# Performance work log

Measured on AMD Instinct MI355X. Metric: run time of the kernel, lower is better.

## Reference

```python
import jax, jax.numpy as jnp
import numpy as np

D = 256
FF = 1024
NH = 8
BZ, TL = 8, 1024
L, Hs, Ws = 1, 64, 64


def _linear(x, w, b):
    # torch nn.Linear convention: w is [out, in]
    return x @ w.T + b


def _ln(x, g, b, eps=1e-5):
    m = x.mean(-1, keepdims=True)
    v = ((x - m) ** 2).mean(-1, keepdims=True)
    return (x - m) / jnp.sqrt(v + eps) * g + b


def setup_inputs() -> dict:
    key = jax.random.key(0)
    ks = jax.random.split(key, 16)
    s = 0.02
    inp = {
        "tgt": jax.random.normal(ks[0], (BZ, TL, D), jnp.float32),
        "reference_points": jax.random.uniform(ks[1], (BZ, TL, 2), jnp.float32),
        "srcs": jax.random.normal(ks[2], (BZ, L, D, Hs, Ws), jnp.float32),
        "posemb_2d": jax.random.normal(ks[3], (BZ, TL, D), jnp.float32),
        # self-attn (nn.MultiheadAttention) params
        "in_proj_w": jax.random.normal(ks[4], (3 * D, D), jnp.float32) * s,
        "in_proj_b": jnp.zeros((3 * D,), jnp.float32),
        "out_proj_w": jax.random.normal(ks[5], (D, D), jnp.float32) * s,
        "out_proj_b": jnp.zeros((D,), jnp.float32),
        # hand-rolled cross-attn linears (q, k, v, out)
        "lin_q_w": jax.random.normal(ks[6], (D, D), jnp.float32) * s,
        "lin_q_b": jnp.zeros((D,), jnp.float32),
        "lin_k_w": jax.random.normal(ks[7], (D, D), jnp.float32) * s,
        "lin_k_b": jnp.zeros((D,), jnp.float32),
        "lin_v_w": jax.random.normal(ks[8], (D, D), jnp.float32) * s,
        "lin_v_b": jnp.zeros((D,), jnp.float32),
        "lin_o_w": jax.random.normal(ks[9], (D, D), jnp.float32) * s,
        "lin_o_b": jnp.zeros((D,), jnp.float32),
        # layer norms
        "norm1_g": jnp.ones((D,), jnp.float32),
        "norm1_b": jnp.zeros((D,), jnp.float32),
        "norm2_g": jnp.ones((D,), jnp.float32),
        "norm2_b": jnp.zeros((D,), jnp.float32),
        # FFN
        "ffn_w1": jax.random.normal(ks[10], (FF, D), jnp.float32) * s,
        "ffn_b1": jnp.zeros((FF,), jnp.float32),
        "ffn_w2": jax.random.normal(ks[11], (D, FF), jnp.float32) * s,
        "ffn_b2": jnp.zeros((D,), jnp.float32),
        "ffn_norm_g": jnp.ones((D,), jnp.float32),
        "ffn_norm_b": jnp.zeros((D,), jnp.float32),
    }
    return inp


def reference(tgt, reference_points, srcs, posemb_2d,
              in_proj_w, in_proj_b, out_proj_w, out_proj_b,
              lin_q_w, lin_q_b, lin_k_w, lin_k_b, lin_v_w, lin_v_b,
              lin_o_w, lin_o_b,
              norm1_g, norm1_b, norm2_g, norm2_b,
              ffn_w1, ffn_b1, ffn_w2, ffn_b2, ffn_norm_g, ffn_norm_b):
    bz, tl, c = tgt.shape
    nh = NH
    dh = c // nh
    scale = dh ** -0.5

    # ---- self-attention (nn.MultiheadAttention math) ----
    qk = tgt + posemb_2d  # q = k = with_pos_embed(tgt, posemb_2d_)
    wq, wk, wv = in_proj_w[:c], in_proj_w[c:2 * c], in_proj_w[2 * c:]
    bq, bk, bv = in_proj_b[:c], in_proj_b[c:2 * c], in_proj_b[2 * c:]
    qp = _linear(qk, wq, bq).reshape(bz, tl, nh, dh)
    kp = _linear(qk, wk, bk).reshape(bz, tl, nh, dh)
    vp = _linear(tgt, wv, bv).reshape(bz, tl, nh, dh)
    att = jax.nn.softmax(jnp.einsum('bqhd,bkhd->bhqk', qp * scale, kp), axis=-1)
    sa = jnp.einsum('bhqk,bkhd->bqhd', att, vp).reshape(bz, tl, c)
    sa = _linear(sa, out_proj_w, out_proj_b)
    tgt = _ln(tgt + sa, norm2_g, norm2_b)

    # ---- hand-rolled cross attention ----
    bz_, l, c_, h, w = srcs.shape
    s = jnp.transpose(srcs.reshape(bz_ * l, c_, h, w), (0, 2, 3, 1)).reshape(bz_ * l, h * w, c_)
    query = _linear(tgt, lin_q_w, lin_q_b)          # [bz, tl, c]
    key = _linear(s, lin_k_w, lin_k_b)              # [bz*l, hw, c]
    value = _linear(s, lin_v_w, lin_v_b)
    affinity = jax.nn.softmax(jnp.einsum('bqc,bkc->bqk', query, key), axis=-1)  # no 1/sqrt(d) scale, faithful
    tgt2 = _linear(jnp.einsum('bqk,bkc->bqc', affinity, value), lin_o_w, lin_o_b)
    tgt = _ln(tgt + tgt2, norm1_g, norm1_b)

    # ---- FFN ----
    src2 = _linear(jax.nn.relu(_linear(tgt, ffn_w1, ffn_b1)), ffn_w2, ffn_b2)
    tgt = _ln(tgt + src2, ffn_norm_g, ffn_norm_b)
    return tgt
```

## Files before the change

kernel.cpp:

```cpp
#include <hip/hip_runtime.h>
#include <hip/hip_bf16.h>
#include <math.h>

typedef __attribute__((ext_vector_type(8))) __bf16 bf16x8;
typedef __attribute__((ext_vector_type(4))) __bf16 bf16x4;
typedef __attribute__((ext_vector_type(2))) __bf16 bf16x2;
typedef __attribute__((ext_vector_type(4))) float  f32x4;

#define MFMA16(a,b,c) __builtin_amdgcn_mfma_f32_16x16x32_bf16((a),(b),(c),0,0,0)

__device__ __forceinline__ unsigned pack2bf(float a, float b){
  bf16x2 t; t[0] = (__bf16)a; t[1] = (__bf16)b;
  return __builtin_bit_cast(unsigned, t);
}
__device__ __forceinline__ int perm1(int r){ return ((r<<2)|(r>>1)) & 7; }

__device__ __forceinline__ bf16x8 cvt8(const float4& a, const float4& b){
  bf16x8 h;
  h[0]=(__bf16)a.x; h[1]=(__bf16)a.y; h[2]=(__bf16)a.z; h[3]=(__bf16)a.w;
  h[4]=(__bf16)b.x; h[5]=(__bf16)b.y; h[6]=(__bf16)b.z; h[7]=(__bf16)b.w;
  return h;
}

template<int BM, bool RELU, int OUTMODE, int AMODE>
__global__ __launch_bounds__(256) void gemm_bt(
    const void* __restrict__ Av, const float* __restrict__ A2,
    const float* __restrict__ W,
    const float* __restrict__ bias, void* __restrict__ Cv,
    int M, int N, int K, int ldc, int coff, float oscale)
{
  constexpr int MT = BM/32;
  constexpr int PASSES = BM/64;
  __shared__ __align__(16) __bf16 As[BM][72];
  __shared__ __align__(16) __bf16 Bs[64][72];

  const int tid  = threadIdx.x;
  const int wid  = tid >> 6;
  const int lane = tid & 63;
  const int wr   = wid >> 1;
  const int wc   = wid & 1;
  const int lq   = lane & 15;
  const int lk8  = (lane >> 4) << 3;
  const int rb   = (lane >> 4) << 2;

  const int m0 = blockIdx.x * BM;
  const int n0 = blockIdx.y * 64;

  const int sr = tid >> 2;
  const int sc = (tid & 3) << 4;

  f32x4 acc[MT][2];
  #pragma unroll
  for (int i=0;i<MT;i++)
    #pragma unroll
    for (int j=0;j<2;j++) acc[i][j] = f32x4{0.f,0.f,0.f,0.f};

  for (int k0=0; k0<K; k0+=64){
    __syncthreads();
    #pragma unroll
    for (int p=0;p<PASSES;p++){
      const int row = sr + p*64;
      if (AMODE == 2){
        const __bf16* ap = (const __bf16*)Av + (size_t)(m0+row)*K + k0 + sc;
        *(bf16x8*)&As[row][sc]   = *(const bf16x8*)(ap);
        *(bf16x8*)&As[row][sc+8] = *(const bf16x8*)(ap + 8);
      } else {
        const float* ap = (const float*)Av + (size_t)(m0+row)*K + k0 + sc;
        float4 a0 = *(const float4*)(ap);
        float4 a1 = *(const float4*)(ap+4);
        float4 a2 = *(const float4*)(ap+8);
        float4 a3 = *(const float4*)(ap+12);
        if (AMODE == 1){
          const float* bp = A2 + (size_t)(m0+row)*K + k0 + sc;
          const float4 b0 = *(const float4*)(bp);
          const float4 b1 = *(const float4*)(bp+4);
          const float4 b2 = *(const float4*)(bp+8);
          const float4 b3 = *(const float4*)(bp+12);
          a0.x+=b0.x; a0.y+=b0.y; a0.z+=b0.z; a0.w+=b0.w;
          a1.x+=b1.x; a1.y+=b1.y; a1.z+=b1.z; a1.w+=b1.w;
          a2.x+=b2.x; a2.y+=b2.y; a2.z+=b2.z; a2.w+=b2.w;
          a3.x+=b3.x; a3.y+=b3.y; a3.z+=b3.z; a3.w+=b3.w;
        }
        *(bf16x8*)&As[row][sc]   = cvt8(a0,a1);
        *(bf16x8*)&As[row][sc+8] = cvt8(a2,a3);
      }
    }
    {
      const float* wp = W + (size_t)(n0+sr)*K + k0 + sc;
      const float4 a0 = *(const float4*)(wp);
      const float4 a1 = *(const float4*)(wp+4);
      const float4 a2 = *(const float4*)(wp+8);
      const float4 a3 = *(const float4*)(wp+12);
      *(bf16x8*)&Bs[sr][sc]   = cvt8(a0,a1);
      *(bf16x8*)&Bs[sr][sc+8] = cvt8(a2,a3);
    }
    __syncthreads();
    #pragma unroll
    for (int ksub=0; ksub<2; ksub++){
      bf16x8 bfr[2];
      #pragma unroll
      for (int j=0;j<2;j++)
        bfr[j] = *(const bf16x8*)&Bs[wc*32 + j*16 + lq][ksub*32 + lk8];
      #pragma unroll
      for (int i=0;i<MT;i++){
        const bf16x8 af = *(const bf16x8*)&As[wr*(BM/2) + i*16 + lq][ksub*32 + lk8];
        acc[i][0] = MFMA16(af, bfr[0], acc[i][0]);
        acc[i][1] = MFMA16(af, bfr[1], acc[i][1]);
      }
    }
  }

  #pragma unroll
  for (int i=0;i<MT;i++)
    #pragma unroll
    for (int j=0;j<2;j++){
      const int coln = n0 + wc*32 + j*16 + lq;
      const float bv = bias ? bias[coln] : 0.f;
      if (OUTMODE == 2){
        const int rowm0 = m0 + wr*(BM/2) + i*16 + rb;
        bf16x4 hv;
        #pragma unroll
        for (int r=0;r<4;r++){
          float vv = (acc[i][j][r] + bv) * oscale;
          if (RELU) vv = fmaxf(vv, 0.f);
          hv[r] = (__bf16)vv;
        }
        *(bf16x4*)&((__bf16*)Cv)[((size_t)((rowm0>>10)*256) + coln)*1024 + (rowm0&1023)] = hv;
      } else {
        #pragma unroll
        for (int r=0;r<4;r++){
          const int rowm = m0 + wr*(BM/2) + i*16 + rb + r;
          float vv = (acc[i][j][r] + bv) * oscale;
          if (RELU) vv = fmaxf(vv, 0.f);
          const size_t idx = (size_t)rowm*ldc + coff + coln;
          if (OUTMODE == 1) ((__bf16*)Cv)[idx] = (__bf16)vv;
          else              ((float*)Cv)[idx]  = vv;
        }
      }
    }
}

template<bool TRANSOUT>
__global__ __launch_bounds__(256) void gemm_srcs(
    const float* __restrict__ S, const float* __restrict__ W,
    const float* __restrict__ bias, __bf16* __restrict__ C)
{
  __shared__ __align__(16) __bf16 As[128][40];
  __shared__ __align__(16) __bf16 Bs[64][40];

  const int tid  = threadIdx.x;
  const int wid  = tid >> 6;
  const int lane = tid & 63;
  const int wr   = wid >> 1;
  const int wc   = wid & 1;
  const int lq   = lane & 15;
  const int lk8  = (lane >> 4) << 3;
  const int rb   = (lane >> 4) << 2;

  const int m0 = blockIdx.x * 128;
  const int n0 = blockIdx.y * 64;
  const int bb = m0 >> 12;
  const int p0 = m0 & 4095;

  const int cA = tid & 31;
  const int qA = tid >> 5;
  const int scg = (tid & 7) << 2;
  const int sr  = tid >> 3;

  f32x4 acc[4][2];
  #pragma unroll
  for (int i=0;i<4;i++)
    #pragma unroll
    for (int j=0;j<2;j++) acc[i][j] = f32x4{0.f,0.f,0.f,0.f};

  for (int k0=0; k0<256; k0+=32){
    __syncthreads();
    const float* sbase = &S[((size_t)bb*256 + k0 + cA)*4096 + p0];
    #pragma unroll
    for (int ps=0; ps<4; ps++){
      const int p = ps*32 + qA*4;
      const float4 f4 = *(const float4*)(sbase + p);
      As[p+0][cA] = (__bf16)f4.x;
      As[p+1][cA] = (__bf16)f4.y;
      As[p+2][cA] = (__bf16)f4.z;
      As[p+3][cA] = (__bf16)f4.w;
    }
    #pragma unroll
    for (int i=0;i<2;i++){
      const int row = sr + i*32;
      const float4 a4 = *(const float4*)&W[(size_t)(n0+row)*256 + k0 + scg];
      bf16x4 h; h[0]=(__bf16)a4.x; h[1]=(__bf16)a4.y; h[2]=(__bf16)a4.z; h[3]=(__bf16)a4.w;
      *(bf16x4*)&Bs[row][scg] = h;
    }
    __syncthreads();
    bf16x8 af[4], bfr[2];
    #pragma unroll
    for (int i=0;i<4;i++) af[i]  = *(const bf16x8*)&As[wr*64 + i*16 + lq][lk8];
    #pragma unroll
    for (int j=0;j<2;j++) bfr[j] = *(const bf16x8*)&Bs[wc*32 + j*16 + lq][lk8];
    #pragma unroll
    for (int i=0;i<4;i++)
      #pragma unroll
      for (int j=0;j<2;j++)
        acc[i][j] = MFMA16(af[i], bfr[j], acc[i][j]);
  }

  #pragma unroll
  for (int i=0;i<4;i++)
    #pragma unroll
    for (int j=0;j<2;j++){
      const int coln = n0 + wc*32 + j*16 + lq;
      const float bv = bias ? bias[coln] : 0.f;
      if (TRANSOUT){
        bf16x4 hv;
        #pragma unroll
        for (int r=0;r<4;r++) hv[r] = (__bf16)(acc[i][j][r] + bv);
        *(bf16x4*)&C[((size_t)bb*256 + coln)*4096 + p0 + wr*64 + i*16 + rb] = hv;
      } else {
        #pragma unroll
        for (int r=0;r<4;r++){
          const int rowm = m0 + wr*64 + i*16 + rb + r;
          C[(size_t)rowm*256 + coln] = (__bf16)(acc[i][j][r] + bv);
        }
      }
    }
}

__global__ __launch_bounds__(256) void ln_kernel(const float* __restrict__ res,
                                                 const float* __restrict__ x,
                                                 const float* __restrict__ g,
                                                 const float* __restrict__ beta,
                                                 float* __restrict__ out,
                                                 __bf16* __restrict__ outb)
{
  const int row  = blockIdx.x*4 + (threadIdx.x >> 6);
  const int lane = threadIdx.x & 63;
  const int c = lane*4;
  const float4 rv = *(const float4*)&res[(size_t)row*256 + c];
  const float4 xv = *(const float4*)&x[(size_t)row*256 + c];
  float v0=rv.x+xv.x, v1=rv.y+xv.y, v2=rv.z+xv.z, v3=rv.w+xv.w;
  float s = v0+v1+v2+v3;
  #pragma unroll
  for (int off=1; off<64; off<<=1) s += __shfl_xor(s, off);
  const float mean = s * (1.f/256.f);
  const float d0=v0-mean, d1=v1-mean, d2=v2-mean, d3=v3-mean;
  float q = d0*d0 + d1*d1 + d2*d2 + d3*d3;
  #pragma unroll
  for (int off=1; off<64; off<<=1) q += __shfl_xor(q, off);
  const float rstd = rsqrtf(q*(1.f/256.f) + 1e-5f);
  const float4 gv = *(const float4*)&g[c];
  const float4 bv = *(const float4*)&beta[c];
  float4 ov;
  ov.x = d0*rstd*gv.x + bv.x;
  ov.y = d1*rstd*gv.y + bv.y;
  ov.z = d2*rstd*gv.z + bv.z;
  ov.w = d3*rstd*gv.w + bv.w;
  *(float4*)&out[(size_t)row*256 + c] = ov;
  if (outb){
    bf16x4 hv;
    hv[0]=(__bf16)ov.x; hv[1]=(__bf16)ov.y; hv[2]=(__bf16)ov.z; hv[3]=(__bf16)ov.w;
    *(bf16x4*)&outb[(size_t)row*256 + c] = hv;
  }
}

__global__ __launch_bounds__(256) void flash_self(
    const __bf16* __restrict__ qks, const __bf16* __restrict__ vts,
    __bf16* __restrict__ sab)
{
  const int qt = blockIdx.x;
  const int b  = blockIdx.y >> 3;
  const int h  = blockIdx.y & 7;
  const int tid  = threadIdx.x;
  const int wid  = tid >> 6;
  const int lane = tid & 63;
  const int lq   = lane & 15;
  const int hi   = lane >> 4;
  const int lk8  = hi << 3;
  const int rb   = hi << 2;
  const float SCALE = 0.17677669529663687f;

  const int qrow = b*1024 + qt*64 + wid*16 + lq;
  const bf16x8 qf = *(const bf16x8*)&qks[(size_t)qrow*512 + h*32 + lk8];

  const __bf16* kb0 = &qks[(size_t)(b*1024 + lq)*512 + 256 + h*32 + lk8];
  const __bf16* vb0 = &vts[(size_t)(b*256 + h*32 + lq)*1024 + lk8];

  const f32x4 Z = {0.f, 0.f, 0.f, 0.f};
  float m = -1e30f, l = 0.f;
  f32x4 o0 = Z, o1 = Z;

  for (int it=0; it<16; ++it){
    const int key0 = it*64;
    f32x4 s4[4];
    #pragma unroll
    for (int kt=0;kt<4;kt++){
      const bf16x8 kf = *(const bf16x8*)(kb0 + (size_t)(key0 + kt*16)*512);
      s4[kt] = MFMA16(kf, qf, Z);
      #pragma unroll
      for (int r=0;r<4;r++) s4[kt][r] *= SCALE;
    }
    float pm = s4[0][0];
    #pragma unroll
    for (int kt=0;kt<4;kt++)
      #pragma unroll
      for (int r=0;r<4;r++) pm = fmaxf(pm, s4[kt][r]);
    pm = fmaxf(pm, __shfl_xor(pm,16));
    pm = fmaxf(pm, __shfl_xor(pm,32));
    if (!__all(pm <= m + 8.f)){
      const float mn = fmaxf(m, pm);
      const float alpha = __expf(m - mn);
      o0[0]*=alpha; o0[1]*=alpha; o0[2]*=alpha; o0[3]*=alpha;
      o1[0]*=alpha; o1[1]*=alpha; o1[2]*=alpha; o1[3]*=alpha;
      l *= alpha;
      m = mn;
    }
    float p[4][4]; float rs = 0.f;
    #pragma unroll
    for (int kt=0;kt<4;kt++)
      #pragma unroll
      for (int r=0;r<4;r++){ p[kt][r] = __expf(s4[kt][r]-m); rs += p[kt][r]; }
    rs += __shfl_xor(rs,16);
    rs += __shfl_xor(rs,32);
    l += rs;
    unsigned pk0[4], pk1[4];
    #pragma unroll
    for (int kt=0;kt<4;kt++){
      pk0[kt] = pack2bf(p[kt][0], p[kt][1]);
      pk1[kt] = pack2bf(p[kt][2], p[kt][3]);
    }
    const int srcA = ((hi&1)<<5) + lq;
    const int srcB = srcA + 16;
    const bool ksel = hi >= 2;
    bf16x8 pf[2];
    #pragma unroll
    for (int ks2=0; ks2<2; ks2++){
      const unsigned a0 = (unsigned)__shfl((int)pk0[2*ks2],   srcA);
      const unsigned a1 = (unsigned)__shfl((int)pk0[2*ks2+1], srcA);
      const unsigned b0 = (unsigned)__shfl((int)pk1[2*ks2],   srcA);
      const unsigned b1 = (unsigned)__shfl((int)pk1[2*ks2+1], srcA);
      const unsigned c0 = (unsigned)__shfl((int)pk0[2*ks2],   srcB);
      const unsigned c1 = (unsigned)__shfl((int)pk0[2*ks2+1], srcB);
      const unsigned d0 = (unsigned)__shfl((int)pk1[2*ks2],   srcB);
      const unsigned d1 = (unsigned)__shfl((int)pk1[2*ks2+1], srcB);
      union { unsigned u[4]; bf16x8 v; } uu;
      uu.u[0] = ksel ? a1 : a0;
      uu.u[1] = ksel ? b1 : b0;
      uu.u[2] = ksel ? c1 : c0;
      uu.u[3] = ksel ? d1 : d0;
      pf[ks2] = uu.v;
    }
    #pragma unroll
    for (int ks2=0; ks2<2; ks2++){
      const bf16x8 vf0 = *(const bf16x8*)(vb0 + key0 + ks2*32);
      const bf16x8 vf1 = *(const bf16x8*)(vb0 + (size_t)16*1024 + key0 + ks2*32);
      o0 = MFMA16(vf0, pf[ks2], o0);
      o1 = MFMA16(vf1, pf[ks2], o1);
    }
  }
  const float inv = 1.f / l;
  bf16x4 w0, w1;
  #pragma unroll
  for (int r=0;r<4;r++){ w0[r] = (__bf16)(o0[r]*inv); w1[r] = (__bf16)(o1[r]*inv); }
  *(bf16x4*)&sab[(size_t)qrow*256 + h*32 + rb]      = w0;
  *(bf16x4*)&sab[(size_t)qrow*256 + h*32 + 16 + rb] = w1;
}

__global__ __launch_bounds__(256, 1) void flash_cross(
    const __bf16* __restrict__ qgm, const __bf16* __restrict__ kg,
    const __bf16* __restrict__ vtg, __bf16* __restrict__ Opart,
    float* __restrict__ ml)
{
  extern __shared__ __bf16 smem[];
  __bf16* Ks = smem;
  __bf16* Vt = smem + 64*256;

  const int bid = blockIdx.x;
  const int xcd = bid & 7;
  const int grp = bid >> 3;
  const int qt  = grp & 7;
  const int pp  = xcd + 8*(grp >> 3);
  const int b   = pp >> 3;
  const int sl  = pp & 7;

  const int tid  = threadIdx.x;
  const int wid  = tid >> 6;
  const int lane = tid & 63;
  const int lq   = lane & 15;
  const int hi   = lane >> 4;
  const int lk8  = hi << 3;
  const int rb   = hi << 2;
  const int p1l  = perm1(lq & 7);

  const int q0 = b*1024 + qt*128 + wid*32;
  bf16x8 qf[2][8];
  #pragma unroll
  for (int g=0; g<2; g++)
    #pragma unroll
    for (int ks=0; ks<8; ks++)
      qf[g][ks] = *(const bf16x8*)&qgm[(size_t)(q0 + g*16 + lq)*256 + ks*32 + lk8];

  const f32x4 Z = {0.f, 0.f, 0.f, 0.f};
  float m[2] = {-1e30f, -1e30f};
  float l[2] = {0.f, 0.f};
  f32x4 o[2][16];
  #pragma unroll
  for (int g=0; g<2; g++)
    #pragma unroll
    for (int nf=0; nf<16; nf++) o[g][nf] = Z;

  const int srow = tid >> 2;
  const int c4   = tid & 3;
  const int p1s  = perm1(srow & 7);

  for (int it=0; it<8; ++it){
    const int key0 = sl*512 + it*64;
    __syncthreads();
    {
      const __bf16* kb = &kg[(size_t)(b*4096 + key0 + srow)*256];
      #pragma unroll
      for (int j=0;j<8;j++){
        const int ch = c4 + j*4;
        *(bf16x8*)&Ks[srow*256 + ((ch ^ p1s)<<3)] = *(const bf16x8*)(kb + ch*8);
      }
    }
    {
      #pragma unroll
      for (int ps=0; ps<4; ps++){
        const int d = srow + ps*64;
        const __bf16* vb = &vtg[(size_t)(b*256 + d)*4096 + key0];
        #pragma unroll
        for (int s2=0;s2<2;s2++){
          const int ch = c4 + s2*4;
          *(bf16x8*)&Vt[d*64 + ((ch ^ p1s)<<3)] = *(const bf16x8*)(vb + ch*8);
        }
      }
    }
    __syncthreads();
    f32x4 s4[2][4];
    #pragma unroll
    for (int g=0; g<2; g++)
      #pragma unroll
      for (int kt=0;kt<4;kt++) s4[g][kt] = Z;
    #pragma unroll
    for (int ks=0; ks<8; ks++){
      #pragma unroll
      for (int kt=0; kt<4; kt++){
        const bf16x8 kf = *(const bf16x8*)&Ks[(kt*16+lq)*256 + (((ks*4+hi) ^ p1l)<<3)];
        s4[0][kt] = MFMA16(kf, qf[0][ks], s4[0][kt]);
        s4[1][kt] = MFMA16(kf, qf[1][ks], s4[1][kt]);
      }
    }
    float pm[2];
    #pragma unroll
    for (int g=0; g<2; g++){
      float v = s4[g][0][0];
      #pragma unroll
      for (int kt=0;kt<4;kt++)
        #pragma unroll
        for (int r=0;r<4;r++) v = fmaxf(v, s4[g][kt][r]);
      v = fmaxf(v, __shfl_xor(v, 16));
      v = fmaxf(v, __shfl_xor(v, 32));
      pm[g] = v;
    }
    const bool need = (pm[0] > m[0] + 8.f) || (pm[1] > m[1] + 8.f);
    if (__any(need)){
      #pragma unroll
      for (int g=0; g<2; g++){
        const float mn = fmaxf(m[g], pm[g]);
        const float alpha = __expf(m[g] - mn);
        #pragma unroll
        for (int nf=0;nf<16;nf++){
          o[g][nf][0]*=alpha; o[g][nf][1]*=alpha;
          o[g][nf][2]*=alpha; o[g][nf][3]*=alpha;
        }
        l[g] *= alpha;
        m[g] = mn;
      }
    }
    bf16x8 pf[2][2];
    #pragma unroll
    for (int g=0; g<2; g++){
      float p[4][4];
      float rs = 0.f;
      #pragma unroll
      for (int kt=0;kt<4;kt++)
        #pragma unroll
        for (int r=0;r<4;r++){ p[kt][r] = __expf(s4[g][kt][r] - m[g]); rs += p[kt][r]; }
      rs += __shfl_xor(rs, 16);
      rs += __shfl_xor(rs, 32);
      l[g] += rs;
      unsigned pk0[4], pk1[4];
      #pragma unroll
      for (int kt=0;kt<4;kt++){
        pk0[kt] = pack2bf(p[kt][0], p[kt][1]);
        pk1[kt] = pack2bf(p[kt][2], p[kt][3]);
      }
      const int srcA = ((hi&1)<<5) + lq;
      const int srcB = srcA + 16;
      const bool ksel = hi >= 2;
      #pragma unroll
      for (int ks2=0; ks2<2; ks2++){
        const unsigned a0 = (unsigned)__shfl((int)pk0[2*ks2],   srcA);
        const unsigned a1 = (unsigned)__shfl((int)pk0[2*ks2+1], srcA);
        const unsigned b0 = (unsigned)__shfl((int)pk1[2*ks2],   srcA);
        const unsigned b1 = (unsigned)__shfl((int)pk1[2*ks2+1], srcA);
        const unsigned c0 = (unsigned)__shfl((int)pk0[2*ks2],   srcB);
        const unsigned c1 = (unsigned)__shfl((int)pk0[2*ks2+1], srcB);
        const unsigned d0 = (unsigned)__shfl((int)pk1[2*ks2],   srcB);
        const unsigned d1 = (unsigned)__shfl((int)pk1[2*ks2+1], srcB);
        union { unsigned u[4]; bf16x8 v; } uu;
        uu.u[0] = ksel ? a1 : a0;
        uu.u[1] = ksel ? b1 : b0;
        uu.u[2] = ksel ? c1 : c0;
        uu.u[3] = ksel ? d1 : d0;
        pf[g][ks2] = uu.v;
      }
    }
    #pragma unroll
    for (int nf=0; nf<16; nf++){
      #pragma unroll
      for (int ks2=0; ks2<2; ks2++){
        const bf16x8 af = *(const bf16x8*)&Vt[(nf*16+lq)*64 + (((ks2*4+hi) ^ p1l)<<3)];
        o[0][nf] = MFMA16(af, pf[0][ks2], o[0][nf]);
        o[1][nf] = MFMA16(af, pf[1][ks2], o[1][nf]);
      }
    }
  }
  #pragma unroll
  for (int g=0; g<2; g++){
    const int row = q0 + g*16 + lq;
    if (hi == 0){
      ml[(size_t)(sl*8192 + row)*2 + 0] = m[g];
      ml[(size_t)(sl*8192 + row)*2 + 1] = l[g];
    }
    #pragma unroll
    for (int nf=0; nf<16; nf++){
      bf16x4 hv;
      #pragma unroll
      for (int r=0;r<4;r++) hv[r] = (__bf16)o[g][nf][r];
      *(bf16x4*)&Opart[(size_t)(sl*8192 + row)*256 + nf*16 + rb] = hv;
    }
  }
}

__global__ __launch_bounds__(256) void combine_kernel(const __bf16* __restrict__ Opart,
                                                      const float* __restrict__ ml,
                                                      __bf16* __restrict__ out)
{
  const int row = blockIdx.x;
  const int d = threadIdx.x;
  float mm[8], ll[8];
  #pragma unroll
  for (int s=0;s<8;s++){
    mm[s] = ml[(size_t)(s*8192+row)*2 + 0];
    ll[s] = ml[(size_t)(s*8192+row)*2 + 1];
  }
  float M = mm[0];
  #pragma unroll
  for (int s=1;s<8;s++) M = fmaxf(M, mm[s]);
  float L = 0.f, acc = 0.f;
  #pragma unroll
  for (int s=0;s<8;s++){
    const float e = __expf(mm[s]-M);
    L   += ll[s]*e;
    acc += e * (float)Opart[(size_t)(s*8192+row)*256 + d];
  }
  out[(size_t)row*256 + d] = (__bf16)(acc / L);
}

extern "C" void kernel_launch(void* const* d_in, const int* in_sizes, int n_in,
                              void* d_out, int out_size, void* d_ws, size_t ws_size,
                              hipStream_t stream)
{
  (void)in_sizes; (void)n_in; (void)out_size; (void)ws_size;
  const float* tgt        = (const float*)d_in[0];
  const float* srcs       = (const float*)d_in[2];
  const float* posemb     = (const float*)d_in[3];
  const float* in_proj_w  = (const float*)d_in[4];
  const float* in_proj_b  = (const float*)d_in[5];
  const float* out_proj_w = (const float*)d_in[6];
  const float* out_proj_b = (const float*)d_in[7];
  const float* lin_q_w    = (const float*)d_in[8];
  const float* lin_q_b    = (const float*)d_in[9];
  const float* lin_k_w    = (const float*)d_in[10];
  const float* lin_k_b    = (const float*)d_in[11];
  const float* lin_v_w    = (const float*)d_in[12];
  const float* lin_v_b    = (const float*)d_in[13];
  const float* lin_o_w    = (const float*)d_in[14];
  const float* lin_o_b    = (const float*)d_in[15];
  const float* norm1_g    = (const float*)d_in[16];
  const float* norm1_b    = (const float*)d_in[17];
  const float* norm2_g    = (const float*)d_in[18];
  const float* norm2_b    = (const float*)d_in[19];
  const float* ffn_w1     = (const float*)d_in[20];
  const float* ffn_b1     = (const float*)d_in[21];
  const float* ffn_w2     = (const float*)d_in[22];
  const float* ffn_b2     = (const float*)d_in[23];
  const float* ffn_norm_g = (const float*)d_in[24];
  const float* ffn_norm_b = (const float*)d_in[25];
  float* out = (float*)d_out;

  char* w = (char*)d_ws;
  const size_t MB = (size_t)1 << 20;
  float*  tgt1    = (float*)(w + 0);
  __bf16* qk_s    = (__bf16*)(w + 8*MB);
  __bf16* query_b = (__bf16*)(w + 8*MB);
  __bf16* tgt1b   = (__bf16*)(w + 12*MB);
  __bf16* attn2   = (__bf16*)(w + 12*MB);
  __bf16* v_t     = (__bf16*)(w + 16*MB);
  __bf16* key_b   = (__bf16*)(w + 16*MB);
  float*  t2proj  = (float*)(w + 16*MB);
  __bf16* sa_b    = (__bf16*)(w + 20*MB);
  float*  saproj  = (float*)(w + 24*MB);
  float*  tgt3    = (float*)(w + 24*MB);
  __bf16* val_t   = (__bf16*)(w + 32*MB);
  __bf16* ffn_h   = (__bf16*)(w + 32*MB);
  __bf16* Opart   = (__bf16*)(w + 48*MB);
  float*  ffn_out = (float*)(w + 48*MB);
  __bf16* tgt3b   = (__bf16*)(w + 56*MB);
  float*  ml      = (float*)(w + 80*MB);

  gemm_bt<64,false,1,1><<<dim3(128,8),256,0,stream>>>(tgt, posemb,
      in_proj_w, in_proj_b, qk_s, 8192,512,256, 512,0, 1.f);
  gemm_bt<64,false,2,0><<<dim3(128,4),256,0,stream>>>(tgt, nullptr,
      in_proj_w + 512*256, in_proj_b + 512, v_t, 8192,256,256, 256,0, 1.f);
  flash_self<<<dim3(16,64),256,0,stream>>>(qk_s, v_t, sa_b);
  gemm_bt<64,false,0,2><<<dim3(128,4),256,0,stream>>>(sa_b, nullptr,
      out_proj_w, out_proj_b, saproj, 8192,256,256, 256,0, 1.f);
  ln_kernel<<<2048,256,0,stream>>>(tgt, saproj, norm2_g, norm2_b, tgt1, tgt1b);

  gemm_bt<64,false,1,2><<<dim3(128,4),256,0,stream>>>(tgt1b, nullptr,
      lin_q_w, lin_q_b, query_b, 8192,256,256, 256,0, 1.f);
  gemm_srcs<false><<<dim3(256,4),256,0,stream>>>(srcs, lin_k_w, lin_k_b, key_b);
  gemm_srcs<true ><<<dim3(256,4),256,0,stream>>>(srcs, lin_v_w, lin_v_b, val_t);
  flash_cross<<<512,256,65536,stream>>>(query_b, key_b, val_t, Opart, ml);
  combine_kernel<<<8192,256,0,stream>>>(Opart, ml, attn2);
  gemm_bt<64,false,0,2><<<dim3(128,4),256,0,stream>>>(attn2, nullptr,
      lin_o_w, lin_o_b, t2proj, 8192,256,256, 256,0, 1.f);
  ln_kernel<<<2048,256,0,stream>>>(tgt1, t2proj, norm1_g, norm1_b, tgt3, tgt3b);

  gemm_bt<128,true,1,2><<<dim3(64,16),256,0,stream>>>(tgt3b, nullptr,
      ffn_w1, ffn_b1, ffn_h, 8192,1024,256, 1024,0, 1.f);
  gemm_bt<64,false,0,2><<<dim3(128,4),256,0,stream>>>(ffn_h, nullptr,
      ffn_w2, ffn_b2, ffn_out, 8192,256,1024, 256,0, 1.f);
  ln_kernel<<<2048,256,0,stream>>>(tgt3, ffn_out, ffn_norm_g, ffn_norm_b, out, nullptr);
}
```

Measured before the change: 293.3 us.

## Fuse K and V srcs projections into one kernel holding full A tile in LDS

Replaces the two separate srcs projection GEMMs (K and V, each tiled over four output-column blocks) with a single kernel. Each block converts its 128-position srcs tile once into LDS and then iterates over all eight 64-column weight tiles for K and V. This removes the repeated reads and bf16 conversion of the large fp32 srcs tensor and one launch. In exchange, only 256 blocks run with about 100KB of LDS each, lowering occupancy and serialising the load phase before compute.

```diff
diff --git a/kernel.cpp b/kernel.cpp
--- a/kernel.cpp
+++ b/kernel.cpp
@@ -140,13 +140,15 @@
     }
 }
 
-template<bool TRANSOUT>
-__global__ __launch_bounds__(256) void gemm_srcs(
-    const float* __restrict__ S, const float* __restrict__ W,
-    const float* __restrict__ bias, __bf16* __restrict__ C)
+__global__ __launch_bounds__(256) void gemm_srcs_kv(
+    const float* __restrict__ S,
+    const float* __restrict__ Wk, const float* __restrict__ bk,
+    const float* __restrict__ Wv, const float* __restrict__ bv,
+    __bf16* __restrict__ Kout, __bf16* __restrict__ Vt)
 {
-  __shared__ __align__(16) __bf16 As[128][40];
-  __shared__ __align__(16) __bf16 Bs[64][40];
+  extern __shared__ __bf16 lds[];
+  __bf16* As = lds;
+  __bf16* Bs = lds + 128*264;
 
   const int tid  = threadIdx.x;
   const int wid  = tid >> 6;
@@ -158,72 +160,85 @@
   const int rb   = (lane >> 4) << 2;
 
   const int m0 = blockIdx.x * 128;
-  const int n0 = blockIdx.y * 64;
   const int bb = m0 >> 12;
   const int p0 = m0 & 4095;
 
   const int cA = tid & 31;
   const int qA = tid >> 5;
-  const int scg = (tid & 7) << 2;
-  const int sr  = tid >> 3;
-
-  f32x4 acc[4][2];
-  #pragma unroll
-  for (int i=0;i<4;i++)
-    #pragma unroll
-    for (int j=0;j<2;j++) acc[i][j] = f32x4{0.f,0.f,0.f,0.f};
-
   for (int k0=0; k0<256; k0+=32){
-    __syncthreads();
     const float* sbase = &S[((size_t)bb*256 + k0 + cA)*4096 + p0];
     #pragma unroll
     for (int ps=0; ps<4; ps++){
       const int p = ps*32 + qA*4;
       const float4 f4 = *(const float4*)(sbase + p);
-      As[p+0][cA] = (__bf16)f4.x;
-      As[p+1][cA] = (__bf16)f4.y;
-      As[p+2][cA] = (__bf16)f4.z;
-      As[p+3][cA] = (__bf16)f4.w;
-    }
-    #pragma unroll
-    for (int i=0;i<2;i++){
-      const int row = sr + i*32;
-      const float4 a4 = *(const float4*)&W[(size_t)(n0+row)*256 + k0 + scg];
-      bf16x4 h; h[0]=(__bf16)a4.x; h[1]=(__bf16)a4.y; h[2]=(__bf16)a4.z; h[3]=(__bf16)a4.w;
-      *(bf16x4*)&Bs[row][scg] = h;
-    }
-    __syncthreads();
-    bf16x8 af[4], bfr[2];
-    #pragma unroll
-    for (int i=0;i<4;i++) af[i]  = *(const bf16x8*)&As[wr*64 + i*16 + lq][lk8];
-    #pragma unroll
-    for (int j=0;j<2;j++) bfr[j] = *(const bf16x8*)&Bs[wc*32 + j*16 + lq][lk8];
-    #pragma unroll
-    for (int i=0;i<4;i++)
-      #pragma unroll
-      for (int j=0;j<2;j++)
-        acc[i][j] = MFMA16(af[i], bfr[j], acc[i][j]);
-  }
-
-  #pragma unroll
-  for (int i=0;i<4;i++)
-    #pragma unroll
-    for (int j=0;j<2;j++){
-      const int coln = n0 + wc*32 + j*16 + lq;
-      const float bv = bias ? bias[coln] : 0.f;
-      if (TRANSOUT){
-        bf16x4 hv;
-        #pragma unroll
-        for (int r=0;r<4;r++) hv[r] = (__bf16)(acc[i][j][r] + bv);
-        *(bf16x4*)&C[((size_t)bb*256 + coln)*4096 + p0 + wr*64 + i*16 + rb] = hv;
-      } else {
-        #pragma unroll
-        for (int r=0;r<4;r++){
-          const int rowm = m0 + wr*64 + i*16 + rb + r;
-          C[(size_t)rowm*256 + coln] = (__bf16)(acc[i][j][r] + bv);
-        }
-      }
-    }
+      As[(p+0)*264 + k0 + cA] = (__bf16)f4.x;
+      As[(p+1)*264 + k0 + cA] = (__bf16)f4.y;
+      As[(p+2)*264 + k0 + cA] = (__bf16)f4.z;
+      As[(p+3)*264 + k0 + cA] = (__bf16)f4.w;
+    }
+  }
+
+  const int sr  = tid >> 2;
+  const int scb = (tid & 3) * 64;
+
+  for (int half=0; half<2; half++){
+    const float* W    = half ? Wv : Wk;
+    const float* bias = half ? bv : bk;
+    for (int nt=0; nt<4; nt++){
+      const int n0 = nt*64;
+      __syncthreads();
+      {
+        const float* wp = W + (size_t)(n0+sr)*256 + scb;
+        #pragma unroll
+        for (int j=0;j<4;j++){
+          const float4 a0 = *(const float4*)(wp + j*16);
+          const float4 a1 = *(const float4*)(wp + j*16 + 4);
+          const float4 a2 = *(const float4*)(wp + j*16 + 8);
+          const float4 a3 = *(const float4*)(wp + j*16 + 12);
+          *(bf16x8*)&Bs[sr*264 + scb + j*16]     = cvt8(a0,a1);
+          *(bf16x8*)&Bs[sr*264 + scb + j*16 + 8] = cvt8(a2,a3);
+        }
+      }
+      __syncthreads();
+      f32x4 acc[4][2];
+      #pragma unroll
+      for (int i=0;i<4;i++)
+        #pragma unroll
+        for (int j=0;j<2;j++) acc[i][j] = f32x4{0.f,0.f,0.f,0.f};
+      #pragma unroll
+      for (int k0=0; k0<256; k0+=32){
+        bf16x8 bfr[2];
+        #pragma unroll
+        for (int j=0;j<2;j++)
+          bfr[j] = *(const bf16x8*)&Bs[(wc*32 + j*16 + lq)*264 + k0 + lk8];
+        #pragma unroll
+        for (int i=0;i<4;i++){
+          const bf16x8 af = *(const bf16x8*)&As[(wr*64 + i*16 + lq)*264 + k0 + lk8];
+          acc[i][0] = MFMA16(af, bfr[0], acc[i][0]);
+          acc[i][1] = MFMA16(af, bfr[1], acc[i][1]);
+        }
+      }
+      #pragma unroll
+      for (int i=0;i<4;i++)
+        #pragma unroll
+        for (int j=0;j<2;j++){
+          const int coln = n0 + wc*32 + j*16 + lq;
+          const float bvv = bias[coln];
+          if (half){
+            bf16x4 hv;
+            #pragma unroll
+            for (int r=0;r<4;r++) hv[r] = (__bf16)(acc[i][j][r] + bvv);
+            *(bf16x4*)&Vt[((size_t)bb*256 + coln)*4096 + p0 + wr*64 + i*16 + rb] = hv;
+          } else {
+            #pragma unroll
+            for (int r=0;r<4;r++){
+              const int rowm = m0 + wr*64 + i*16 + rb + r;
+              Kout[(size_t)rowm*256 + coln] = (__bf16)(acc[i][j][r] + bvv);
+            }
+          }
+        }
+    }
+  }
 }
 
 __global__ __launch_bounds__(256) void ln_kernel(const float* __restrict__ res,
@@ -631,8 +646,8 @@
 
   gemm_bt<64,false,1,2><<<dim3(128,4),256,0,stream>>>(tgt1b, nullptr,
       lin_q_w, lin_q_b, query_b, 8192,256,256, 256,0, 1.f);
-  gemm_srcs<false><<<dim3(256,4),256,0,stream>>>(srcs, lin_k_w, lin_k_b, key_b);
-  gemm_srcs<true ><<<dim3(256,4),256,0,stream>>>(srcs, lin_v_w, lin_v_b, val_t);
+  gemm_srcs_kv<<<256,256,(128+64)*264*2,stream>>>(srcs,
+      lin_k_w, lin_k_b, lin_v_w, lin_v_b, key_b, val_t);
   flash_cross<<<512,256,65536,stream>>>(query_b, key_b, val_t, Opart, ml);
   combine_kernel<<<8192,256,0,stream>>>(Opart, ml, attn2);
   gemm_bt<64,false,0,2><<<dim3(128,4),256,0,stream>>>(attn2, nullptr,
```

New measurement: 286.5 us. 1.02x faster.
